# Performance work log

Hardware: AMD Instinct MI355X
Metric: run time of the kernel (lower is better)

The kernel has to match this reference:

```python
import jax, jax.numpy as jnp
import numpy as np
import math

NLAT, NLON, LMAX, MMAX = 128, 256, 50, 50
K = 3  # three_nn

# ---- precompute: Clenshaw-Curtis quadrature (torch_harmonics 'equiangular') ----
def _cc_nodes_weights(n):
    Nn = n - 1
    theta = np.pi * np.arange(n) / Nn
    v = np.zeros(n)
    for k in range(1, Nn // 2 + 1):
        b = 1.0 if 2 * k == Nn else 2.0
        v += b * np.cos(2 * k * theta) / (4 * k * k - 1)
    w = (2.0 / Nn) * (1.0 - v)
    w[0] *= 0.5
    w[-1] *= 0.5
    return np.cos(theta), w

# ---- precompute: orthonormal associated Legendre P_l^m(cos theta), csphase ----
def _legpoly(lmax, mmax, cost):
    sint = np.sqrt(np.clip(1.0 - cost ** 2, 0.0, None))
    p = np.zeros((mmax, lmax, cost.shape[0]))
    pmm = np.full(cost.shape[0], np.sqrt(1.0 / (4.0 * np.pi)))
    for m in range(mmax):
        if m > 0:
            pmm = -pmm * np.sqrt((2.0 * m + 1.0) / (2.0 * m)) * sint
        p[m, m] = pmm
        if m + 1 < lmax:
            p[m, m + 1] = np.sqrt(2.0 * m + 3.0) * cost * pmm
        for l in range(m + 2, lmax):
            a = np.sqrt((4.0 * l * l - 1.0) / (l * l - m * m))
            b = np.sqrt(((2.0 * l + 1.0) * (l - 1 + m) * (l - 1 - m)) / ((2.0 * l - 3.0) * (l * l - m * m)))
            p[m, l] = a * cost * p[m, l - 1] - b * p[m, l - 2]
    return p

_cost, _w = _cc_nodes_weights(NLAT)
_PCTW = jnp.asarray((_legpoly(LMAX, MMAX, _cost) * _w[None, None, :]).astype(np.float32))  # (mmax,lmax,nlat)

_gx, _gy = np.meshgrid(np.arange(NLAT), np.arange(-NLAT, NLAT), indexing='ij')
_GRID = jnp.asarray((np.stack([_gx.ravel(), _gy.ravel()], -1) / NLAT * np.pi).astype(np.float32))  # (M,2)

_RECTW = jnp.asarray(np.exp(-(LMAX - np.arange(1, LMAX + 1)) ** 2 / (2.0 * LMAX ** 2)).astype(np.float32))  # (lmax,)


def to_spherical(coords):
    # coords: (B,N,3) -> r:(B,N), sph:(B,N,2) = [arccos(x/r), azimuth in [0,2pi)]
    sq = coords ** 2
    pn = jnp.sqrt(jnp.flip(jnp.cumsum(jnp.flip(sq, -1), -1), -1))  # pn[...,i] = ||coords[...,i:]||
    r = pn[..., 0]
    phi = jnp.arccos(coords[..., :-2] / pn[..., :-2])
    a = jnp.arccos(coords[..., -2] / pn[..., -2])
    phi_final = a + (2.0 * math.pi - 2.0 * a) * (coords[..., -1] < 0)
    return r, jnp.concatenate([phi, phi_final[..., None]], axis=-1)


def interp_to_grid(coords):
    # spherical transform + 3-NN (squared dists) + distance-weighted interpolation onto the lat/lon grid
    r, sph = to_spherical(coords)
    sph = sph.at[..., 1].add(-math.pi)
    # brute-force pairwise squared distances grid(M,2) vs sph(B,N,2): (B,M,N)
    d2 = (jnp.sum(_GRID ** 2, -1)[None, :, None] + jnp.sum(sph ** 2, -1)[:, None, :]
          - 2.0 * jnp.einsum('md,bnd->bmn', _GRID, sph))
    _, idx = jax.lax.top_k(-jax.lax.stop_gradient(d2), K)  # (B,M,K), ascending distance
    sel = jax.vmap(lambda s, i: s[i])(sph, idx)            # (B,M,K,2)
    fsel = jax.vmap(lambda f, i: f[i])(r, idx)             # (B,M,K)
    dk = jnp.sum((_GRID[None, :, None, :] - sel) ** 2, -1)  # recompute selected sq-dists (differentiable)
    w = dk / jnp.sum(dk, -1, keepdims=True)                # weights = dist / sum(dist), as in source
    return jnp.sum(fsel * w, -1).reshape(-1, NLAT, NLON)


def sht_real(x):
    # RealSHT (equiangular, ortho): rfft(norm='forward')*2pi, then Legendre*quadrature einsum; real part only
    xf = jnp.fft.rfft(x, axis=-1)[..., :MMAX] * (2.0 * math.pi / NLON)
    return jnp.einsum('bkm,mlk->blm', jnp.real(xf).astype(jnp.float32), _PCTW)  # (B,lmax,mmax)


def setup_inputs() -> dict:
    key = jax.random.key(0)
    k1, k2 = jax.random.split(key)
    pred = jax.random.normal(k1, (2, 2048, 3), dtype=jnp.float32)
    target = jax.random.normal(k2, (2, 2048, 3), dtype=jnp.float32)
    return {"pred": pred, "target": target}


def reference(pred, target):
    pc = sht_real(interp_to_grid(pred))
    tc = sht_real(interp_to_grid(target))
    return jnp.mean(jnp.sum((pc - tc) ** 2 * _RECTW[None, :, None], axis=(1, 2)))
```

## Files before the change

kernel.cpp:

```cpp
#include <hip/hip_runtime.h>
#include <math.h>

#define PI_D 3.14159265358979323846
#define PIF  3.14159265358979323846f
#define NLAT 128
#define NLON 256
#define LMAX 50
#define MMAX 50
#define NPTS 2048
#define NBT 16
#define NBA 32
#define NBIN (NBT * NBA)
#define WBIN 0.19634954084936207f
#define INVW 5.092958178940651f
#define BIG 1e30f
#define KMASK 0xFFFFF800u

__device__ __forceinline__ void insert3(float kf, float& k0, float& k1, float& k2) {
    float n1 = __builtin_amdgcn_fmed3f(kf, k0, k1);
    float n2 = __builtin_amdgcn_fmed3f(kf, k1, k2);
    k0 = fminf(kf, k0);
    k1 = n1;
    k2 = n2;
}

__device__ __forceinline__ float mkkey(float gt, float gl, float2 tl, int idx) {
    float dt = gt - tl.x, dl = gl - tl.y;
    float d = fmaf(dt, dt, dl * dl);
    return __uint_as_float((__float_as_uint(d) & KMASK) | (unsigned)idx);
}

__global__ __launch_bounds__(256) void fused_main(
    const float* __restrict__ pred, const float* __restrict__ tgt,
    float* __restrict__ pctwT, float* __restrict__ fre, float* __restrict__ out) {

    __shared__ float2 s_btl[NPTS];
    __shared__ float  s_br[NPTS];
    __shared__ int    s_cnt[NBIN];
    __shared__ int    s_off[NBIN + 1];
    __shared__ float  row[NLON];
    __shared__ float  part[256];

    int bid = blockIdx.x;
    int t = threadIdx.x;

    if (bid >= 256) {
        int k = bid - 256;
        int m = t;
        if (k == 0 && m == 0) out[0] = 0.0f;
        if (m >= MMAX) return;

        double thd = PI_D * (double)k / 127.0;
        float cost = (float)cos(thd);
        float sint = (float)sin(thd);

        float c2 = (float)cos(2.0 * thd);
        float two_c2 = 2.0f * c2;
        float cp = 1.0f, cc = c2, v = 0.0f;
        for (int tt = 1; tt <= 63; ++tt) {
            v += 2.0f * cc / (float)(4 * tt * tt - 1);
            float cn = two_c2 * cc - cp;
            cp = cc;
            cc = cn;
        }
        float w = (2.0f / 127.0f) * (1.0f - v);
        if (k == 0 || k == 127) w *= 0.5f;

        float pmm = sqrtf(1.0f / (4.0f * PIF));
        for (int i = 1; i <= m; ++i)
            pmm = -pmm * sqrtf((2.0f * (float)i + 1.0f) / (2.0f * (float)i)) * sint;

        float* o = pctwT + (size_t)k * MMAX + m;
        for (int l = 0; l < m; ++l) o[(size_t)l * NLAT * MMAX] = 0.0f;
        o[(size_t)m * NLAT * MMAX] = pmm * w;
        float plm2 = pmm, plm1 = 0.0f;
        if (m + 1 < LMAX) {
            plm1 = sqrtf(2.0f * (float)m + 3.0f) * cost * pmm;
            o[(size_t)(m + 1) * NLAT * MMAX] = plm1 * w;
        }
        for (int l = m + 2; l < LMAX; ++l) {
            float fl = (float)l;
            float denom = fl * fl - (float)(m * m);
            float a = sqrtf((4.0f * fl * fl - 1.0f) / denom);
            float b = sqrtf(((2.0f * fl + 1.0f) * (float)(l - 1 + m) * (float)(l - 1 - m)) /
                            ((2.0f * fl - 3.0f) * denom));
            float p = a * cost * plm1 - b * plm2;
            o[(size_t)l * NLAT * MMAX] = p * w;
            plm2 = plm1;
            plm1 = p;
        }
        return;
    }

    int f = bid >> 6;
    int lat0 = (bid & 63) * 2;
    const float* src = ((f < 2) ? pred : tgt) + (size_t)(f & 1) * NPTS * 3;

    s_cnt[t] = 0;
    s_cnt[t + 256] = 0;
    __syncthreads();

    float pth[8], paz[8], pr[8];
    int pbin[8];
#pragma unroll
    for (int i = 0; i < 8; ++i) {
        int n = t + 256 * i;
        float x = src[3 * n], y = src[3 * n + 1], z = src[3 * n + 2];
        float s1 = z * z;
        float s2 = s1 + y * y;
        float s3 = s2 + x * x;
        float r = sqrtf(s3);
        float rho = sqrtf(s2);
        float th = acosf(x / r);
        float a = acosf(y / rho);
        float az = (z < 0.0f) ? (a + (2.0f * PIF - 2.0f * a)) : a;
        az -= PIF;
        int bt = min(max((int)(th * INVW), 0), NBT - 1);
        int ba = min(max((int)((az + PIF) * INVW), 0), NBA - 1);
        int b = bt * NBA + ba;
        pth[i] = th; paz[i] = az; pr[i] = r; pbin[i] = b;
        atomicAdd(&s_cnt[b], 1);
    }
    __syncthreads();

    if (t == 0) s_off[NBIN] = NPTS;
    if (t < 64) {
        int base = t * 8;
        int loc[8];
        int run = 0;
#pragma unroll
        for (int i = 0; i < 8; ++i) { loc[i] = run; run += s_cnt[base + i]; }
        int x = run;
#pragma unroll
        for (int d = 1; d < 64; d <<= 1) {
            int y = __shfl_up(x, d);
            if (t >= d) x += y;
        }
        int ex = x - run;
#pragma unroll
        for (int i = 0; i < 8; ++i) s_off[base + i] = ex + loc[i];
    }
    __syncthreads();
    s_cnt[t] = s_off[t];
    s_cnt[t + 256] = s_off[t + 256];
    __syncthreads();
#pragma unroll
    for (int i = 0; i < 8; ++i) {
        int pos = atomicAdd(&s_cnt[pbin[i]], 1);
        s_btl[pos] = make_float2(pth[i], paz[i]);
        s_br[pos] = pr[i];
    }
    __syncthreads();

    int j = t;
    float gl = (float)(((double)j - 128.0) * PI_D / 128.0);
    float glp = gl + PIF;
    int ba0 = j >> 3;

    for (int rr = 0; rr < 2; ++rr) {
        int lat = lat0 + rr;
        float gt = (float)((double)lat * PI_D / 128.0);
        int bt0 = lat >> 3;

        auto scan_seg = [&](int i, int i1, float& q0, float& q1, float& q2) {
            for (; i + 4 <= i1; i += 4) {
                float2 a0 = s_btl[i];
                float2 a1 = s_btl[i + 1];
                float2 a2 = s_btl[i + 2];
                float2 a3 = s_btl[i + 3];
                insert3(mkkey(gt, gl, a0, i), q0, q1, q2);
                insert3(mkkey(gt, gl, a1, i + 1), q0, q1, q2);
                insert3(mkkey(gt, gl, a2, i + 2), q0, q1, q2);
                insert3(mkkey(gt, gl, a3, i + 3), q0, q1, q2);
            }
            for (; i < i1; ++i)
                insert3(mkkey(gt, gl, s_btl[i], i), q0, q1, q2);
        };

        float k0 = BIG, k1 = BIG, k2 = BIG;
        {
            int rtl = max(bt0 - 1, 0), rth = min(bt0 + 1, NBT - 1);
            int bal = max(ba0 - 1, 0), bah = min(ba0 + 1, NBA - 1);
            for (int bt = rtl; bt <= rth; ++bt)
                scan_seg(s_off[bt * NBA + bal], s_off[bt * NBA + bah + 1], k0, k1, k2);
        }

        bool done;
        {
            float safe = BIG;
            if (bt0 - 1 > 0)       safe = fminf(safe, gt - (float)(bt0 - 1) * WBIN);
            if (bt0 + 1 < NBT - 1) safe = fminf(safe, (float)(bt0 + 2) * WBIN - gt);
            if (ba0 - 1 > 0)       safe = fminf(safe, glp - (float)(ba0 - 1) * WBIN);
            if (ba0 + 1 < NBA - 1) safe = fminf(safe, (float)(ba0 + 2) * WBIN - glp);
            done = (k2 <= safe * safe);
        }

        for (int R = 2; R <= 31; ++R) {
            if (__all(done)) break;
            if (!done) {
                int btl = bt0 - R, bth = bt0 + R;
                int lo = max(btl, 0), hi = min(bth, NBT - 1);
                int bal = max(ba0 - R, 0), bah = min(ba0 + R, NBA - 1);
                for (int bt = lo; bt <= hi; ++bt) {
                    if (bt == btl || bt == bth) {
                        scan_seg(s_off[bt * NBA + bal], s_off[bt * NBA + bah + 1], k0, k1, k2);
                    } else {
                        if (ba0 - R >= 0) {
                            int b = bt * NBA + ba0 - R;
                            scan_seg(s_off[b], s_off[b + 1], k0, k1, k2);
                        }
                        if (ba0 + R <= NBA - 1) {
                            int b = bt * NBA + ba0 + R;
                            scan_seg(s_off[b], s_off[b + 1], k0, k1, k2);
                        }
                    }
                }
                float safe = BIG;
                if (bt0 - R > 0)       safe = fminf(safe, gt - (float)(bt0 - R) * WBIN);
                if (bt0 + R < NBT - 1) safe = fminf(safe, (float)(bt0 + R + 1) * WBIN - gt);
                if (ba0 - R > 0)       safe = fminf(safe, glp - (float)(ba0 - R) * WBIN);
                if (ba0 + R < NBA - 1) safe = fminf(safe, (float)(ba0 + R + 1) * WBIN - glp);
                if (k2 <= safe * safe) done = true;
            }
        }

        {
            int i0 = __float_as_uint(k0) & 0x7FF;
            int i1 = __float_as_uint(k1) & 0x7FF;
            int i2 = __float_as_uint(k2) & 0x7FF;
            float2 p0 = s_btl[i0];
            float2 p1 = s_btl[i1];
            float2 p2 = s_btl[i2];
            float dt0 = gt - p0.x, dl0 = gl - p0.y;
            float dt1 = gt - p1.x, dl1 = gl - p1.y;
            float dt2 = gt - p2.x, dl2 = gl - p2.y;
            float d0 = fmaf(dt0, dt0, dl0 * dl0);
            float d1 = fmaf(dt1, dt1, dl1 * dl1);
            float d2 = fmaf(dt2, dt2, dl2 * dl2);
            float s = d0 + d1 + d2;
            row[j] = (d0 * s_br[i0] + d1 * s_br[i1] + d2 * s_br[i2]) / s;
        }
        __syncthreads();

        {
            int q = t >> 6;
            int mm = t & 63;
            if (mm < MMAX) {
                int bs = q * 64;
                const float W0 = 2.0f * PIF / 256.0f;
                float cphi2 = 2.0f * __cosf(W0 * (float)mm);
                float acc = 0.0f;
#pragma unroll
                for (int seg = 0; seg < 4; ++seg) {
                    int i0 = bs + seg * 16;
                    float c0 = __cosf(W0 * (float)((i0 * mm) & 255));
                    float c1 = __cosf(W0 * (float)(((i0 + 1) * mm) & 255));
                    acc = fmaf(row[i0], c0, acc);
                    acc = fmaf(row[i0 + 1], c1, acc);
#pragma unroll
                    for (int i = 2; i < 16; ++i) {
                        float cn = fmaf(cphi2, c1, -c0);
                        acc = fmaf(row[i0 + i], cn, acc);
                        c0 = c1;
                        c1 = cn;
                    }
                }
                part[q * 64 + mm] = acc;
            }
        }
        __syncthreads();
        if (t < MMAX) {
            float v = ((part[t] + part[64 + t]) + (part[128 + t] + part[192 + t])) *
                      (float)(2.0 * PI_D / (double)NLON);
            fre[(f * NLAT + lat) * MMAX + t] = v;
        }
        __syncthreads();
    }
}

__global__ __launch_bounds__(256) void contract_loss(const float* __restrict__ fre,
                                                     const float* __restrict__ pctwT,
                                                     float* __restrict__ out) {
    int b = blockIdx.x / LMAX;
    int l = blockIdx.x % LMAX;
    int mm = threadIdx.x & 63;
    int kq = threadIdx.x >> 6;
    __shared__ float sp[4][64], st_[4][64];
    float pc = 0.0f, tc = 0.0f;
    if (mm < MMAX) {
        const float* pw = pctwT + ((size_t)l * NLAT + kq * 32) * MMAX + mm;
        const float* fp = fre + ((size_t)b * NLAT + kq * 32) * MMAX + mm;
        const float* ft = fre + ((size_t)(2 + b) * NLAT + kq * 32) * MMAX + mm;
#pragma unroll 8
        for (int k = 0; k < 32; ++k) {
            float w = pw[k * MMAX];
            pc += fp[k * MMAX] * w;
            tc += ft[k * MMAX] * w;
        }
    }
    sp[kq][mm] = pc;
    st_[kq][mm] = tc;
    __syncthreads();
    if (threadIdx.x < 64) {
        int m2 = threadIdx.x;
        float pcs = (sp[0][m2] + sp[1][m2]) + (sp[2][m2] + sp[3][m2]);
        float tcs = (st_[0][m2] + st_[1][m2]) + (st_[2][m2] + st_[3][m2]);
        float diff = pcs - tcs;
        double dl_ = (double)(49 - l);
        float rw = (float)exp(-(dl_ * dl_) / 5000.0);
        float contrib = (m2 < MMAX) ? diff * diff * rw * 0.5f : 0.0f;
        for (int off = 32; off > 0; off >>= 1) contrib += __shfl_down(contrib, off);
        if (m2 == 0) atomicAdd(out, contrib);
    }
}

extern "C" void kernel_launch(void* const* d_in, const int* in_sizes, int n_in,
                              void* d_out, int out_size, void* d_ws, size_t ws_size,
                              hipStream_t stream) {
    const float* pred = (const float*)d_in[0];
    const float* tgt = (const float*)d_in[1];
    float* ws = (float*)d_ws;

    float* pctwT = ws;
    float* fre   = ws + 320000;
    float* out = (float*)d_out;

    fused_main<<<384, 256, 0, stream>>>(pred, tgt, pctwT, fre, out);
    contract_loss<<<2 * LMAX, 256, 0, stream>>>(fre, pctwT, out);
}
```

Baseline: 82.11 us.

## Process four latitude rows per 1024-thread block to share point binning

Each main block now runs 1024 threads and handles four latitude rows at once, one row per 256-thread group, instead of 256 threads looping over two rows. The block grid shrinks from 256 to 128 main blocks plus the Legendre blocks. Each block still rebuilds the binned point set from all 2048 points, so the total redundant binning work is halved and its per-thread cost is spread over more threads. The trade-offs are lower block count and occupancy, a wider `__syncthreads` scope, and Legendre blocks that now launch 1024 threads while using only 50.

```diff
diff --git a/kernel.cpp b/kernel.cpp
--- a/kernel.cpp
+++ b/kernel.cpp
@@ -30,7 +30,7 @@
     return __uint_as_float((__float_as_uint(d) & KMASK) | (unsigned)idx);
 }
 
-__global__ __launch_bounds__(256) void fused_main(
+__global__ __launch_bounds__(1024) void fused_main(
     const float* __restrict__ pred, const float* __restrict__ tgt,
     float* __restrict__ pctwT, float* __restrict__ fre, float* __restrict__ out) {
 
@@ -38,14 +38,14 @@
     __shared__ float  s_br[NPTS];
     __shared__ int    s_cnt[NBIN];
     __shared__ int    s_off[NBIN + 1];
-    __shared__ float  row[NLON];
-    __shared__ float  part[256];
+    __shared__ float  s_row[4][NLON];
+    __shared__ float  s_part[4][256];
 
     int bid = blockIdx.x;
     int t = threadIdx.x;
 
-    if (bid >= 256) {
-        int k = bid - 256;
+    if (bid >= 128) {
+        int k = bid - 128;
         int m = t;
         if (k == 0 && m == 0) out[0] = 0.0f;
         if (m >= MMAX) return;
@@ -92,19 +92,18 @@
         return;
     }
 
-    int f = bid >> 6;
-    int lat0 = (bid & 63) * 2;
+    int f = bid >> 5;
+    int lat0 = (bid & 31) * 4;
     const float* src = ((f < 2) ? pred : tgt) + (size_t)(f & 1) * NPTS * 3;
 
-    s_cnt[t] = 0;
-    s_cnt[t + 256] = 0;
-    __syncthreads();
-
-    float pth[8], paz[8], pr[8];
-    int pbin[8];
-#pragma unroll
-    for (int i = 0; i < 8; ++i) {
-        int n = t + 256 * i;
+    if (t < NBIN) s_cnt[t] = 0;
+    __syncthreads();
+
+    float pth[2], paz[2], pr[2];
+    int pbin[2];
+#pragma unroll
+    for (int i = 0; i < 2; ++i) {
+        int n = t + 1024 * i;
         float x = src[3 * n], y = src[3 * n + 1], z = src[3 * n + 2];
         float s1 = z * z;
         float s2 = s1 + y * y;
@@ -141,140 +140,140 @@
         for (int i = 0; i < 8; ++i) s_off[base + i] = ex + loc[i];
     }
     __syncthreads();
-    s_cnt[t] = s_off[t];
-    s_cnt[t + 256] = s_off[t + 256];
-    __syncthreads();
-#pragma unroll
-    for (int i = 0; i < 8; ++i) {
+    if (t < NBIN) s_cnt[t] = s_off[t];
+    __syncthreads();
+#pragma unroll
+    for (int i = 0; i < 2; ++i) {
         int pos = atomicAdd(&s_cnt[pbin[i]], 1);
         s_btl[pos] = make_float2(pth[i], paz[i]);
         s_br[pos] = pr[i];
     }
     __syncthreads();
 
-    int j = t;
+    int rl = t >> 8;
+    int j = t & 255;
+    int lat = lat0 + rl;
+    float gt = (float)((double)lat * PI_D / 128.0);
     float gl = (float)(((double)j - 128.0) * PI_D / 128.0);
     float glp = gl + PIF;
+    int bt0 = lat >> 3;
     int ba0 = j >> 3;
 
-    for (int rr = 0; rr < 2; ++rr) {
-        int lat = lat0 + rr;
-        float gt = (float)((double)lat * PI_D / 128.0);
-        int bt0 = lat >> 3;
-
-        auto scan_seg = [&](int i, int i1, float& q0, float& q1, float& q2) {
-            for (; i + 4 <= i1; i += 4) {
-                float2 a0 = s_btl[i];
-                float2 a1 = s_btl[i + 1];
-                float2 a2 = s_btl[i + 2];
-                float2 a3 = s_btl[i + 3];
-                insert3(mkkey(gt, gl, a0, i), q0, q1, q2);
-                insert3(mkkey(gt, gl, a1, i + 1), q0, q1, q2);
-                insert3(mkkey(gt, gl, a2, i + 2), q0, q1, q2);
-                insert3(mkkey(gt, gl, a3, i + 3), q0, q1, q2);
-            }
-            for (; i < i1; ++i)
-                insert3(mkkey(gt, gl, s_btl[i], i), q0, q1, q2);
-        };
-
-        float k0 = BIG, k1 = BIG, k2 = BIG;
-        {
-            int rtl = max(bt0 - 1, 0), rth = min(bt0 + 1, NBT - 1);
-            int bal = max(ba0 - 1, 0), bah = min(ba0 + 1, NBA - 1);
-            for (int bt = rtl; bt <= rth; ++bt)
-                scan_seg(s_off[bt * NBA + bal], s_off[bt * NBA + bah + 1], k0, k1, k2);
-        }
-
-        bool done;
-        {
-            float safe = BIG;
-            if (bt0 - 1 > 0)       safe = fminf(safe, gt - (float)(bt0 - 1) * WBIN);
-            if (bt0 + 1 < NBT - 1) safe = fminf(safe, (float)(bt0 + 2) * WBIN - gt);
-            if (ba0 - 1 > 0)       safe = fminf(safe, glp - (float)(ba0 - 1) * WBIN);
-            if (ba0 + 1 < NBA - 1) safe = fminf(safe, (float)(ba0 + 2) * WBIN - glp);
-            done = (k2 <= safe * safe);
-        }
-
-        for (int R = 2; R <= 31; ++R) {
-            if (__all(done)) break;
-            if (!done) {
-                int btl = bt0 - R, bth = bt0 + R;
-                int lo = max(btl, 0), hi = min(bth, NBT - 1);
-                int bal = max(ba0 - R, 0), bah = min(ba0 + R, NBA - 1);
-                for (int bt = lo; bt <= hi; ++bt) {
-                    if (bt == btl || bt == bth) {
-                        scan_seg(s_off[bt * NBA + bal], s_off[bt * NBA + bah + 1], k0, k1, k2);
-                    } else {
-                        if (ba0 - R >= 0) {
-                            int b = bt * NBA + ba0 - R;
-                            scan_seg(s_off[b], s_off[b + 1], k0, k1, k2);
-                        }
-                        if (ba0 + R <= NBA - 1) {
-                            int b = bt * NBA + ba0 + R;
-                            scan_seg(s_off[b], s_off[b + 1], k0, k1, k2);
-                        }
+    auto scan_seg = [&](int i, int i1, float& q0, float& q1, float& q2) {
+        for (; i + 4 <= i1; i += 4) {
+            float2 a0 = s_btl[i];
+            float2 a1 = s_btl[i + 1];
+            float2 a2 = s_btl[i + 2];
+            float2 a3 = s_btl[i + 3];
+            insert3(mkkey(gt, gl, a0, i), q0, q1, q2);
+            insert3(mkkey(gt, gl, a1, i + 1), q0, q1, q2);
+            insert3(mkkey(gt, gl, a2, i + 2), q0, q1, q2);
+            insert3(mkkey(gt, gl, a3, i + 3), q0, q1, q2);
+        }
+        for (; i < i1; ++i)
+            insert3(mkkey(gt, gl, s_btl[i], i), q0, q1, q2);
+    };
+
+    float k0 = BIG, k1 = BIG, k2 = BIG;
+    {
+        int rtl = max(bt0 - 1, 0), rth = min(bt0 + 1, NBT - 1);
+        int bal = max(ba0 - 1, 0), bah = min(ba0 + 1, NBA - 1);
+        for (int bt = rtl; bt <= rth; ++bt)
+            scan_seg(s_off[bt * NBA + bal], s_off[bt * NBA + bah + 1], k0, k1, k2);
+    }
+
+    bool done;
+    {
+        float safe = BIG;
+        if (bt0 - 1 > 0)       safe = fminf(safe, gt - (float)(bt0 - 1) * WBIN);
+        if (bt0 + 1 < NBT - 1) safe = fminf(safe, (float)(bt0 + 2) * WBIN - gt);
+        if (ba0 - 1 > 0)       safe = fminf(safe, glp - (float)(ba0 - 1) * WBIN);
+        if (ba0 + 1 < NBA - 1) safe = fminf(safe, (float)(ba0 + 2) * WBIN - glp);
+        done = (k2 <= safe * safe);
+    }
+
+    for (int R = 2; R <= 31; ++R) {
+        if (__all(done)) break;
+        if (!done) {
+            int btl = bt0 - R, bth = bt0 + R;
+            int lo = max(btl, 0), hi = min(bth, NBT - 1);
+            int bal = max(ba0 - R, 0), bah = min(ba0 + R, NBA - 1);
+            for (int bt = lo; bt <= hi; ++bt) {
+                if (bt == btl || bt == bth) {
+                    scan_seg(s_off[bt * NBA + bal], s_off[bt * NBA + bah + 1], k0, k1, k2);
+                } else {
+                    if (ba0 - R >= 0) {
+                        int b = bt * NBA + ba0 - R;
+                        scan_seg(s_off[b], s_off[b + 1], k0, k1, k2);
+                    }
+                    if (ba0 + R <= NBA - 1) {
+                        int b = bt * NBA + ba0 + R;
+                        scan_seg(s_off[b], s_off[b + 1], k0, k1, k2);
                     }
                 }
-                float safe = BIG;
-                if (bt0 - R > 0)       safe = fminf(safe, gt - (float)(bt0 - R) * WBIN);
-                if (bt0 + R < NBT - 1) safe = fminf(safe, (float)(bt0 + R + 1) * WBIN - gt);
-                if (ba0 - R > 0)       safe = fminf(safe, glp - (float)(ba0 - R) * WBIN);
-                if (ba0 + R < NBA - 1) safe = fminf(safe, (float)(ba0 + R + 1) * WBIN - glp);
-                if (k2 <= safe * safe) done = true;
             }
-        }
-
-        {
-            int i0 = __float_as_uint(k0) & 0x7FF;
-            int i1 = __float_as_uint(k1) & 0x7FF;
-            int i2 = __float_as_uint(k2) & 0x7FF;
-            float2 p0 = s_btl[i0];
-            float2 p1 = s_btl[i1];
-            float2 p2 = s_btl[i2];
-            float dt0 = gt - p0.x, dl0 = gl - p0.y;
-            float dt1 = gt - p1.x, dl1 = gl - p1.y;
-            float dt2 = gt - p2.x, dl2 = gl - p2.y;
-            float d0 = fmaf(dt0, dt0, dl0 * dl0);
-            float d1 = fmaf(dt1, dt1, dl1 * dl1);
-            float d2 = fmaf(dt2, dt2, dl2 * dl2);
-            float s = d0 + d1 + d2;
-            row[j] = (d0 * s_br[i0] + d1 * s_br[i1] + d2 * s_br[i2]) / s;
-        }
-        __syncthreads();
-
-        {
-            int q = t >> 6;
-            int mm = t & 63;
-            if (mm < MMAX) {
-                int bs = q * 64;
-                const float W0 = 2.0f * PIF / 256.0f;
-                float cphi2 = 2.0f * __cosf(W0 * (float)mm);
-                float acc = 0.0f;
-#pragma unroll
-                for (int seg = 0; seg < 4; ++seg) {
-                    int i0 = bs + seg * 16;
-                    float c0 = __cosf(W0 * (float)((i0 * mm) & 255));
-                    float c1 = __cosf(W0 * (float)(((i0 + 1) * mm) & 255));
-                    acc = fmaf(row[i0], c0, acc);
-                    acc = fmaf(row[i0 + 1], c1, acc);
-#pragma unroll
-                    for (int i = 2; i < 16; ++i) {
-                        float cn = fmaf(cphi2, c1, -c0);
-                        acc = fmaf(row[i0 + i], cn, acc);
-                        c0 = c1;
-                        c1 = cn;
-                    }
+            float safe = BIG;
+            if (bt0 - R > 0)       safe = fminf(safe, gt - (float)(bt0 - R) * WBIN);
+            if (bt0 + R < NBT - 1) safe = fminf(safe, (float)(bt0 + R + 1) * WBIN - gt);
+            if (ba0 - R > 0)       safe = fminf(safe, glp - (float)(ba0 - R) * WBIN);
+            if (ba0 + R < NBA - 1) safe = fminf(safe, (float)(ba0 + R + 1) * WBIN - glp);
+            if (k2 <= safe * safe) done = true;
+        }
+    }
+
+    {
+        int i0 = __float_as_uint(k0) & 0x7FF;
+        int i1 = __float_as_uint(k1) & 0x7FF;
+        int i2 = __float_as_uint(k2) & 0x7FF;
+        float2 p0 = s_btl[i0];
+        float2 p1 = s_btl[i1];
+        float2 p2 = s_btl[i2];
+        float dt0 = gt - p0.x, dl0 = gl - p0.y;
+        float dt1 = gt - p1.x, dl1 = gl - p1.y;
+        float dt2 = gt - p2.x, dl2 = gl - p2.y;
+        float d0 = fmaf(dt0, dt0, dl0 * dl0);
+        float d1 = fmaf(dt1, dt1, dl1 * dl1);
+        float d2 = fmaf(dt2, dt2, dl2 * dl2);
+        float s = d0 + d1 + d2;
+        s_row[rl][j] = (d0 * s_br[i0] + d1 * s_br[i1] + d2 * s_br[i2]) / s;
+    }
+    __syncthreads();
+
+    {
+        int q = (t >> 6) & 3;
+        int mm = t & 63;
+        if (mm < MMAX) {
+            int bs = q * 64;
+            const float W0 = 2.0f * PIF / 256.0f;
+            float cphi2 = 2.0f * __cosf(W0 * (float)mm);
+            float acc = 0.0f;
+#pragma unroll
+            for (int seg = 0; seg < 4; ++seg) {
+                int i0 = bs + seg * 16;
+                float c0 = __cosf(W0 * (float)((i0 * mm) & 255));
+                float c1 = __cosf(W0 * (float)(((i0 + 1) * mm) & 255));
+                acc = fmaf(s_row[rl][i0], c0, acc);
+                acc = fmaf(s_row[rl][i0 + 1], c1, acc);
+#pragma unroll
+                for (int i = 2; i < 16; ++i) {
+                    float cn = fmaf(cphi2, c1, -c0);
+                    acc = fmaf(s_row[rl][i0 + i], cn, acc);
+                    c0 = c1;
+                    c1 = cn;
                 }
-                part[q * 64 + mm] = acc;
             }
-        }
-        __syncthreads();
-        if (t < MMAX) {
-            float v = ((part[t] + part[64 + t]) + (part[128 + t] + part[192 + t])) *
+            s_part[rl][q * 64 + mm] = acc;
+        }
+    }
+    __syncthreads();
+    {
+        int mm = t & 255;
+        if (mm < MMAX) {
+            const float* pp = s_part[rl];
+            float v = ((pp[mm] + pp[64 + mm]) + (pp[128 + mm] + pp[192 + mm])) *
                       (float)(2.0 * PI_D / (double)NLON);
-            fre[(f * NLAT + lat) * MMAX + t] = v;
-        }
-        __syncthreads();
+            fre[(f * NLAT + lat0 + rl) * MMAX + mm] = v;
+        }
     }
 }
 
@@ -325,6 +324,6 @@
     float* fre   = ws + 320000;
     float* out = (float*)d_out;
 
-    fused_main<<<384, 256, 0, stream>>>(pred, tgt, pctwT, fre, out);
+    fused_main<<<256, 1024, 0, stream>>>(pred, tgt, pctwT, fre, out);
     contract_loss<<<2 * LMAX, 256, 0, stream>>>(fre, pctwT, out);
 }
```

Measured after the change: 78.48 us, median of 2. 1.05x faster.
